# Performance work log

Measured on AMD Instinct MI355X. Metric: run time of the kernel, lower is better.

## Reference

```python
import jax, jax.numpy as jnp
import numpy as np

N = 100000      # num nodes
E = 1600000     # num edges (avg degree 16)
D_IN = 128
D_OUT = 128
EPS = 1e-12     # F.normalize default eps


def setup_inputs() -> dict:
    key = jax.random.key(0)
    k1, k2, k3, k4 = jax.random.split(key, 4)
    x = jax.random.normal(k1, (N, D_IN), dtype=jnp.float32)
    row = jax.random.randint(k2, (E,), 0, N, dtype=jnp.int32)
    # guarantee no self loops in the raw graph: col = (row + offset) % N, offset in [1, N)
    offset = jax.random.randint(k3, (E,), 1, N, dtype=jnp.int32)
    col = (row + offset) % N
    edge_index = jnp.stack([row, col], axis=0)
    # xavier_uniform_ for weight [in, out]
    a = np.sqrt(6.0 / (D_IN + D_OUT)).astype(np.float32)
    weight = jax.random.uniform(k4, (D_IN, D_OUT), dtype=jnp.float32, minval=-a, maxval=a)
    return {"x": x, "edge_index": edge_index, "weight": weight}


def reference(x, edge_index, weight):
    row, col = edge_index[0], edge_index[1]
    # remove_self_loops: drop edges with row == col (mask keeps shapes static)
    mask = (row != col)
    # linear transform first (as in the original forward)
    xw = jnp.matmul(x, weight)                               # [N, D_OUT]
    # scatter_mean over edges with self loops added:
    # out[i] = (sum_{j->i, j!=i} xw[j] + xw[i]) / (deg_nonself(i) + 1)
    msg = jnp.where(mask[:, None], xw[col], jnp.float32(0.0))  # [E, D_OUT]
    seg_sum = jax.ops.segment_sum(msg, row, num_segments=N) + xw
    cnt = jax.ops.segment_sum(mask.astype(xw.dtype), row, num_segments=N) + jnp.float32(1.0)
    out = seg_sum / cnt[:, None]
    # F.normalize(out, p=2, dim=-1): out / max(||out||_2, eps)
    norm = jnp.sqrt(jnp.sum(out * out, axis=-1, keepdims=True))
    out = out / jnp.maximum(norm, jnp.float32(EPS))
    return out
```

## Files before the change

### kernel.cpp

```cpp
#include <hip/hip_runtime.h>
#include <hip/hip_fp16.h>
#include <stdint.h>

#define NN 100000
#define NE 1600000
#define DD 128

#define NBKT 391
#define CAPB 4480
#define NBIN 3125
#define GCAP 1024

typedef _Float16 f16x8 __attribute__((ext_vector_type(8)));
typedef float f32x4 __attribute__((ext_vector_type(4)));

__device__ __forceinline__ uint32_t hadd2u(uint32_t a, uint32_t b){
  union { uint32_t u; __half2 h; } x, y;
  x.u = a; y.u = b;
  x.h = __hadd2(x.h, y.h);
  return x.u;
}
__device__ __forceinline__ uint32_t hmul2u(uint32_t a, __half2 m){
  union { uint32_t u; __half2 h; } x; x.u = a;
  x.h = __hmul2(x.h, m);
  return x.u;
}

__global__ __launch_bounds__(256) void k_front(
    const int* __restrict__ ei, int* __restrict__ bktres, uint32_t* __restrict__ ibuf,
    const float4* __restrict__ x, uint2* __restrict__ x16,
    const float* __restrict__ w, uint16_t* __restrict__ wsw){
  int b = blockIdx.x, t = threadIdx.x;
  if (b < NBKT){
    __shared__ int sh[NBKT];
    int e0 = b*4096;
    for (int i=t; i<NBKT; i+=256) sh[i] = 0;
    __syncthreads();
    int rr[16], cc[16];
    #pragma unroll
    for (int j=0;j<16;j++){
      int e = e0 + j*256 + t;
      rr[j] = -1;
      if (e < NE){
        rr[j] = ei[e]; cc[j] = ei[NE + e];
        atomicAdd(&sh[rr[j] >> 8], 1);
      }
    }
    __syncthreads();
    for (int i=t; i<NBKT; i+=256){
      int v = sh[i];
      sh[i] = v ? atomicAdd(&bktres[i*16], v) : 0;
    }
    __syncthreads();
    #pragma unroll
    for (int j=0;j<16;j++){
      if (rr[j] >= 0){
        int bk = rr[j] >> 8;
        int p = atomicAdd(&sh[bk], 1);
        if (p < CAPB)
          ibuf[(size_t)bk*CAPB + p] = (uint32_t)(((rr[j] & 255) << 17) | cc[j]);
      }
    }
  } else if (b < 12891){
    int i = (b - NBKT)*256 + t;
    float4 v = x[i];
    union { _Float16 h[4]; uint2 u; } r;
    r.h[0] = (_Float16)v.x; r.h[1] = (_Float16)v.y;
    r.h[2] = (_Float16)v.z; r.h[3] = (_Float16)v.w;
    x16[i] = r.u;
  } else {
    int wi = (b - 12891)*256 + t;
    int j = wi & 7, l = (wi >> 3) & 63, kt = (wi >> 9) & 3, ct = wi >> 11;
    int k = kt*32 + ((l >> 4) & 3)*8 + j;
    int d = ct*16 + (l & 15);
    union { _Float16 h; uint16_t u; } cv; cv.h = (_Float16)w[k*DD + d];
    wsw[wi] = cv.u;
  }
}

__global__ __launch_bounds__(256) void k_part2(const int* __restrict__ bktres,
                                               uint32_t* __restrict__ ibuf,
                                               uint32_t* __restrict__ rowinfo){
  __shared__ uint32_t s_rec[CAPB];
  __shared__ int s_deg[256], s_off[256], s_cur[256];
  int t = threadIdx.x, lane = t & 63, wid = t >> 6;
  int b = blockIdx.x;
  int cnt = bktres[b*16]; if (cnt > CAPB) cnt = CAPB;
  size_t bb = (size_t)b*CAPB;
  s_deg[t] = 0;
  __syncthreads();
  for (int i=t; i<cnt; i+=256){
    uint32_t rec = ibuf[bb + i];
    s_rec[i] = rec;
    atomicAdd(&s_deg[rec >> 17], 1);
  }
  __syncthreads();
  if (wid == 0){
    int carry = 0;
    for (int ch=0; ch<4; ch++){
      int idx = ch*64 + lane;
      int o = s_deg[idx], v = o;
      #pragma unroll
      for (int d=1; d<64; d<<=1){ int y = __shfl_up(v, d); if (lane >= d) v += y; }
      int ex = carry + v - o;
      s_off[idx] = ex; s_cur[idx] = ex;
      carry += __shfl(v, 63);
    }
  }
  __syncthreads();
  int dgc = s_deg[t] > 255 ? 255 : s_deg[t];
  rowinfo[b*256 + t] = ((uint32_t)s_off[t] << 8) | (uint32_t)dgc;
  for (int i=t; i<cnt; i+=256){
    uint32_t rec = s_rec[i];
    int p = atomicAdd(&s_cur[rec >> 17], 1);
    ibuf[bb + p] = rec & 0x1FFFFu;
  }
}

__global__ __launch_bounds__(256) void k_gather_gemm(
    const uint2* __restrict__ xp, const uint32_t* __restrict__ ibuf,
    const uint32_t* __restrict__ rowinfo, const uint16_t* __restrict__ wsw,
    float* __restrict__ out){
  __shared__ int s_col[GCAP];
  __shared__ int s_loc[32], s_deg[32];
  __shared__ uint16_t sAgg[4096];
  __shared__ float sSq[2][2][4][4];
  int t = threadIdx.x, wid = t >> 6, lane = t & 63;
  int b = blockIdx.x;
  int row0 = b << 5;
  if (t < 32){
    uint32_t info = rowinfo[row0 + t];
    s_loc[t] = (int)(info >> 8);
    s_deg[t] = (int)(info & 255u);
  }
  __syncthreads();
  int base = s_loc[0];
  int len = s_loc[31] + s_deg[31] - base; if (len > GCAP) len = GCAP;
  size_t bb = (size_t)(row0 >> 8)*CAPB + base;
  for (int i=t; i<len; i+=256) s_col[i] = (int)ibuf[bb + i];
  __syncthreads();

  int q = lane & 31, half = lane >> 5;
  for (int lr = wid; lr < 32; lr += 4){
    int n = row0 + lr;
    int dg  = s_deg[lr];
    int off = s_loc[lr] - base;
    uint2 sv = xp[(size_t)n*32 + q];
    uint32_t a01 = 0u, a23 = 0u;
    int j = 0;
    for (; j+32 <= dg; j += 32){
      int cI[16];
      #pragma unroll
      for (int u=0; u<16; u++) cI[u] = s_col[off + j + 2*u + half];
      uint2 vI[16];
      #pragma unroll
      for (int u=0; u<16; u++) vI[u] = xp[(size_t)cI[u]*32 + q];
      #pragma unroll
      for (int u=0; u<16; u++){ a01 = hadd2u(a01, vI[u].x); a23 = hadd2u(a23, vI[u].y); }
    }
    for (; j+8 <= dg; j += 8){
      int c0 = s_col[off+j+half],   c1 = s_col[off+j+2+half];
      int c2 = s_col[off+j+4+half], c3 = s_col[off+j+6+half];
      uint2 v0 = xp[(size_t)c0*32 + q]; uint2 v1 = xp[(size_t)c1*32 + q];
      uint2 v2 = xp[(size_t)c2*32 + q]; uint2 v3 = xp[(size_t)c3*32 + q];
      a01 = hadd2u(a01, v0.x); a23 = hadd2u(a23, v0.y);
      a01 = hadd2u(a01, v1.x); a23 = hadd2u(a23, v1.y);
      a01 = hadd2u(a01, v2.x); a23 = hadd2u(a23, v2.y);
      a01 = hadd2u(a01, v3.x); a23 = hadd2u(a23, v3.y);
    }
    for (; j+2 <= dg; j += 2){
      int c0 = s_col[off+j+half];
      uint2 v0 = xp[(size_t)c0*32 + q];
      a01 = hadd2u(a01, v0.x); a23 = hadd2u(a23, v0.y);
    }
    if (j < dg){
      int c0 = s_col[off+j];
      uint2 v0 = xp[(size_t)c0*32 + q];
      a01 = hadd2u(a01, half ? 0u : v0.x);
      a23 = hadd2u(a23, half ? 0u : v0.y);
    }
    a01 = hadd2u(a01, (uint32_t)__shfl_xor((int)a01, 32));
    a23 = hadd2u(a23, (uint32_t)__shfl_xor((int)a23, 32));
    __half2 inv2 = __float2half2_rn(1.0f / (float)(dg + 1));
    uint32_t r01 = hmul2u(hadd2u(a01, sv.x), inv2);
    uint32_t r23 = hmul2u(hadd2u(a23, sv.y), inv2);
    uint32_t pair = half ? r23 : r01;
    int k0 = q*4 + half*2;
    int kt = k0 >> 5, gk = (k0 >> 3) & 3, jj = k0 & 7;
    int ld = (lr & 15) + (gk << 4);
    int lg = lr >> 4;
    *(uint32_t*)&sAgg[((lg*4 + kt)*64 + ld)*8 + jj] = pair;
  }
  __syncthreads();

  int g2 = wid >> 1, ch = (wid & 1)*4;
  const f16x8* Bf = (const f16x8*)wsw;
  f16x8 a0 = *(const f16x8*)&sAgg[((g2*4+0)*64 + lane)*8];
  f16x8 a1 = *(const f16x8*)&sAgg[((g2*4+1)*64 + lane)*8];
  f16x8 a2 = *(const f16x8*)&sAgg[((g2*4+2)*64 + lane)*8];
  f16x8 a3 = *(const f16x8*)&sAgg[((g2*4+3)*64 + lane)*8];
  f32x4 acc[4];
  #pragma unroll
  for (int c2=0;c2<4;c2++) acc[c2] = (f32x4){0.f,0.f,0.f,0.f};
  #pragma unroll
  for (int c2=0;c2<4;c2++){
    acc[c2] = __builtin_amdgcn_mfma_f32_16x16x32_f16(a0, Bf[((ch+c2)*4+0)*64 + lane], acc[c2], 0, 0, 0);
    acc[c2] = __builtin_amdgcn_mfma_f32_16x16x32_f16(a1, Bf[((ch+c2)*4+1)*64 + lane], acc[c2], 0, 0, 0);
    acc[c2] = __builtin_amdgcn_mfma_f32_16x16x32_f16(a2, Bf[((ch+c2)*4+2)*64 + lane], acc[c2], 0, 0, 0);
    acc[c2] = __builtin_amdgcn_mfma_f32_16x16x32_f16(a3, Bf[((ch+c2)*4+3)*64 + lane], acc[c2], 0, 0, 0);
  }
  float sq[4] = {0.f,0.f,0.f,0.f};
  #pragma unroll
  for (int c2=0;c2<4;c2++){
    #pragma unroll
    for (int i=0;i<4;i++) sq[i] += acc[c2][i]*acc[c2][i];
  }
  #pragma unroll
  for (int m=1;m<16;m<<=1){
    #pragma unroll
    for (int i=0;i<4;i++) sq[i] += __shfl_xor(sq[i], m);
  }
  if ((lane & 15) == 0){
    #pragma unroll
    for (int i=0;i<4;i++) sSq[g2][wid & 1][lane >> 4][i] = sq[i];
  }
  __syncthreads();
  float sc[4];
  #pragma unroll
  for (int i=0;i<4;i++){
    float tot = sq[i] + sSq[g2][(wid & 1) ^ 1][lane >> 4][i];
    sc[i] = 1.0f / fmaxf(sqrtf(tot), 1e-12f);
  }
  int col = lane & 15;
  int rb = row0 + g2*16 + ((lane >> 4) << 2);
  #pragma unroll
  for (int i=0;i<4;i++){
    int n = rb + i;
    #pragma unroll
    for (int c2=0;c2<4;c2++)
      out[(size_t)n*DD + (ch + c2)*16 + col] = acc[c2][i]*sc[i];
  }
}

extern "C" void kernel_launch(void* const* d_in, const int* in_sizes, int n_in,
                              void* d_out, int out_size, void* d_ws, size_t ws_size,
                              hipStream_t stream){
  const float* x = (const float*)d_in[0];
  const int*  ei = (const int*)d_in[1];
  const float* w = (const float*)d_in[2];
  float* out = (float*)d_out;
  char* ws = (char*)d_ws;
  (void)in_sizes; (void)n_in; (void)out_size; (void)ws_size;

  size_t off = 0;
  uint16_t* x16 = (uint16_t*)(ws + off); off += (size_t)NN*DD*2;
  uint16_t* wsw = (uint16_t*)(ws + off); off += (size_t)DD*DD*2;
  uint32_t* ibuf = (uint32_t*)(ws + off); off += (size_t)NBKT*CAPB*4;
  int* bktres   = (int*)(ws + off); off += (size_t)NBKT*16*4;
  uint32_t* rowinfo = (uint32_t*)(ws + off); off += (size_t)NBKT*256*4;

  hipMemsetAsync(bktres, 0, (size_t)NBKT*16*4, stream);
  k_front<<<12955, 256, 0, stream>>>(ei, bktres, ibuf, (const float4*)x, (uint2*)x16, w, wsw);
  k_part2<<<NBKT, 256, 0, stream>>>(bktres, ibuf, rowinfo);
  k_gather_gemm<<<NBIN, 256, 0, stream>>>((const uint2*)x16, ibuf, rowinfo, wsw, out);
}
```

Before: 139.0 us.

## Shrink gather-GEMM blocks to 16 rows with 2 waves and swizzled LDS

The gather+GEMM kernel now processes 16 rows per block using 128 threads, doubling the grid. Each wave computes the full 128 output columns for the 16 rows, so the cross-wave sum-of-squares exchange and its extra barrier go away. The LDS staging of aggregated rows uses an XOR swizzle to reduce bank conflicts. The 32-wide unrolled gather loop is dropped, and launch bounds request 6 blocks per CU. The aim is higher occupancy and less synchronisation, at the cost of less memory-level parallelism per wave and each wave reading the whole weight matrix.

Result: no change. 136.4 us (-1.9%).

```diff
diff --git a/kernel.cpp b/kernel.cpp
--- a/kernel.cpp
+++ b/kernel.cpp
@@ -8,8 +8,8 @@
 
 #define NBKT 391
 #define CAPB 4480
-#define NBIN 3125
-#define GCAP 1024
+#define NBIN 6250
+#define GCAP 512
 
 typedef _Float16 f16x8 __attribute__((ext_vector_type(8)));
 typedef float f32x4 __attribute__((ext_vector_type(4)));
@@ -117,47 +117,36 @@
   }
 }
 
-__global__ __launch_bounds__(256) void k_gather_gemm(
+__global__ __launch_bounds__(128, 6) void k_gather_gemm(
     const uint2* __restrict__ xp, const uint32_t* __restrict__ ibuf,
     const uint32_t* __restrict__ rowinfo, const uint16_t* __restrict__ wsw,
     float* __restrict__ out){
   __shared__ int s_col[GCAP];
-  __shared__ int s_loc[32], s_deg[32];
-  __shared__ uint16_t sAgg[4096];
-  __shared__ float sSq[2][2][4][4];
+  __shared__ int s_loc[16], s_deg[16];
+  __shared__ uint32_t sAgg[1024];
   int t = threadIdx.x, wid = t >> 6, lane = t & 63;
   int b = blockIdx.x;
-  int row0 = b << 5;
-  if (t < 32){
+  int row0 = b << 4;
+  if (t < 16){
     uint32_t info = rowinfo[row0 + t];
     s_loc[t] = (int)(info >> 8);
     s_deg[t] = (int)(info & 255u);
   }
   __syncthreads();
   int base = s_loc[0];
-  int len = s_loc[31] + s_deg[31] - base; if (len > GCAP) len = GCAP;
+  int len = s_loc[15] + s_deg[15] - base; if (len > GCAP) len = GCAP;
   size_t bb = (size_t)(row0 >> 8)*CAPB + base;
-  for (int i=t; i<len; i+=256) s_col[i] = (int)ibuf[bb + i];
+  for (int i=t; i<len; i+=128) s_col[i] = (int)ibuf[bb + i];
   __syncthreads();
 
   int q = lane & 31, half = lane >> 5;
-  for (int lr = wid; lr < 32; lr += 4){
+  for (int lr = wid; lr < 16; lr += 2){
     int n = row0 + lr;
     int dg  = s_deg[lr];
     int off = s_loc[lr] - base;
     uint2 sv = xp[(size_t)n*32 + q];
     uint32_t a01 = 0u, a23 = 0u;
     int j = 0;
-    for (; j+32 <= dg; j += 32){
-      int cI[16];
-      #pragma unroll
-      for (int u=0; u<16; u++) cI[u] = s_col[off + j + 2*u + half];
-      uint2 vI[16];
-      #pragma unroll
-      for (int u=0; u<16; u++) vI[u] = xp[(size_t)cI[u]*32 + q];
-      #pragma unroll
-      for (int u=0; u<16; u++){ a01 = hadd2u(a01, vI[u].x); a23 = hadd2u(a23, vI[u].y); }
-    }
     for (; j+8 <= dg; j += 8){
       int c0 = s_col[off+j+half],   c1 = s_col[off+j+2+half];
       int c2 = s_col[off+j+4+half], c3 = s_col[off+j+6+half];
@@ -187,58 +176,52 @@
     uint32_t pair = half ? r23 : r01;
     int k0 = q*4 + half*2;
     int kt = k0 >> 5, gk = (k0 >> 3) & 3, jj = k0 & 7;
-    int ld = (lr & 15) + (gk << 4);
-    int lg = lr >> 4;
-    *(uint32_t*)&sAgg[((lg*4 + kt)*64 + ld)*8 + jj] = pair;
-  }
-  __syncthreads();
-
-  int g2 = wid >> 1, ch = (wid & 1)*4;
+    int ld = lr + (gk << 4);
+    int wdx = (kt*64 + ld)*4 + (jj >> 1);
+    wdx ^= (kt << 3) ^ ((gk & 1) << 2);
+    sAgg[wdx] = pair;
+  }
+  __syncthreads();
+
   const f16x8* Bf = (const f16x8*)wsw;
-  f16x8 a0 = *(const f16x8*)&sAgg[((g2*4+0)*64 + lane)*8];
-  f16x8 a1 = *(const f16x8*)&sAgg[((g2*4+1)*64 + lane)*8];
-  f16x8 a2 = *(const f16x8*)&sAgg[((g2*4+2)*64 + lane)*8];
-  f16x8 a3 = *(const f16x8*)&sAgg[((g2*4+3)*64 + lane)*8];
-  f32x4 acc[4];
-  #pragma unroll
-  for (int c2=0;c2<4;c2++) acc[c2] = (f32x4){0.f,0.f,0.f,0.f};
-  #pragma unroll
-  for (int c2=0;c2<4;c2++){
-    acc[c2] = __builtin_amdgcn_mfma_f32_16x16x32_f16(a0, Bf[((ch+c2)*4+0)*64 + lane], acc[c2], 0, 0, 0);
-    acc[c2] = __builtin_amdgcn_mfma_f32_16x16x32_f16(a1, Bf[((ch+c2)*4+1)*64 + lane], acc[c2], 0, 0, 0);
-    acc[c2] = __builtin_amdgcn_mfma_f32_16x16x32_f16(a2, Bf[((ch+c2)*4+2)*64 + lane], acc[c2], 0, 0, 0);
-    acc[c2] = __builtin_amdgcn_mfma_f32_16x16x32_f16(a3, Bf[((ch+c2)*4+3)*64 + lane], acc[c2], 0, 0, 0);
+  f16x8 a[4];
+  #pragma unroll
+  for (int kt=0; kt<4; kt++){
+    int wb = ((kt*64 + lane)*4) ^ (kt << 3) ^ (((lane >> 4) & 1) << 2);
+    a[kt] = *(const f16x8*)&sAgg[wb];
+  }
+  f32x4 acc[8];
+  #pragma unroll
+  for (int ct=0;ct<8;ct++) acc[ct] = (f32x4){0.f,0.f,0.f,0.f};
+  #pragma unroll
+  for (int ct=0;ct<8;ct++){
+    #pragma unroll
+    for (int kt=0;kt<4;kt++)
+      acc[ct] = __builtin_amdgcn_mfma_f32_16x16x32_f16(a[kt], Bf[(ct*4+kt)*64 + lane], acc[ct], 0, 0, 0);
   }
   float sq[4] = {0.f,0.f,0.f,0.f};
   #pragma unroll
-  for (int c2=0;c2<4;c2++){
-    #pragma unroll
-    for (int i=0;i<4;i++) sq[i] += acc[c2][i]*acc[c2][i];
+  for (int ct=0;ct<8;ct++){
+    #pragma unroll
+    for (int i=0;i<4;i++) sq[i] += acc[ct][i]*acc[ct][i];
   }
   #pragma unroll
   for (int m=1;m<16;m<<=1){
     #pragma unroll
     for (int i=0;i<4;i++) sq[i] += __shfl_xor(sq[i], m);
   }
-  if ((lane & 15) == 0){
-    #pragma unroll
-    for (int i=0;i<4;i++) sSq[g2][wid & 1][lane >> 4][i] = sq[i];
-  }
-  __syncthreads();
   float sc[4];
   #pragma unroll
-  for (int i=0;i<4;i++){
-    float tot = sq[i] + sSq[g2][(wid & 1) ^ 1][lane >> 4][i];
-    sc[i] = 1.0f / fmaxf(sqrtf(tot), 1e-12f);
-  }
+  for (int i=0;i<4;i++) sc[i] = 1.0f / fmaxf(sqrtf(sq[i]), 1e-12f);
+
   int col = lane & 15;
-  int rb = row0 + g2*16 + ((lane >> 4) << 2);
+  int rb = row0 + ((lane >> 4) << 2);
   #pragma unroll
   for (int i=0;i<4;i++){
     int n = rb + i;
     #pragma unroll
-    for (int c2=0;c2<4;c2++)
-      out[(size_t)n*DD + (ch + c2)*16 + col] = acc[c2][i]*sc[i];
+    for (int ct=0;ct<8;ct++)
+      out[(size_t)n*DD + (ct<<4) + col] = acc[ct][i]*sc[i];
   }
 }
 
@@ -262,5 +245,5 @@
   hipMemsetAsync(bktres, 0, (size_t)NBKT*16*4, stream);
   k_front<<<12955, 256, 0, stream>>>(ei, bktres, ibuf, (const float4*)x, (uint2*)x16, w, wsw);
   k_part2<<<NBKT, 256, 0, stream>>>(bktres, ibuf, rowinfo);
-  k_gather_gemm<<<NBIN, 256, 0, stream>>>((const uint2*)x16, ibuf, rowinfo, wsw, out);
-}
+  k_gather_gemm<<<NBIN, 128, 0, stream>>>((const uint2*)x16, ibuf, rowinfo, wsw, out);
+}
```
